# Kernel tuning notes

Measured on AMD Instinct MI355X. Metric: run time of the kernel, lower is better.

Reference implementation:

```python
import jax, jax.numpy as jnp
import numpy as np

B, V, H, W = 2, 16, 512, 512
MAX_VARS, EMBED, P = 48, 1024, 8


def setup_inputs() -> dict:
    key = jax.random.key(0)
    k1, k2, k3, k4 = jax.random.split(key, 4)
    x = jax.random.normal(k1, (B, V, H, W), dtype=jnp.float32)
    vars_idx = jax.random.randint(k2, (V,), 0, MAX_VARS)
    # params scaled roughly like kaiming_uniform for fan_in = P*P
    bound = 1.0 / np.sqrt(P * P)
    proj_weights = jax.random.normal(k3, (MAX_VARS, EMBED, 1, P, P), dtype=jnp.float32) * bound
    proj_biases = jax.random.normal(k4, (MAX_VARS, EMBED), dtype=jnp.float32) * bound
    return {"x": x, "vars": vars_idx, "proj_weights": proj_weights, "proj_biases": proj_biases}


def reference(x, vars, proj_weights, proj_biases):
    # x: [B, V, H, W]; proj_weights: [max_vars, E, 1, p, p]; proj_biases: [max_vars, E]
    b, v, h_img, w_img = x.shape
    p = proj_weights.shape[-1]
    w_sel = proj_weights[vars][:, :, 0]          # [V, E, p, p]  (weight gather)
    b_sel = proj_biases[vars]                    # [V, E]
    hh, ww = h_img // p, w_img // p
    # non-overlapping patch extraction (stride == kernel) + per-variable matmul
    xp = x.reshape(b, v, hh, p, ww, p)           # [B, V, hh, p, ww, p]
    proj = jnp.einsum('bvhpwq,vepq->bvhwe', xp, w_sel)  # [B, V, hh, ww, E]
    # flatten=True: [B, V, L, E], L = hh*ww (matches reshape->flatten(3)->transpose(2,3))
    out = proj.reshape(b, v, hh * ww, -1) + b_sel[None, :, None, :]
    return out  # norm_layer=None -> Identity
```

## Files before the change

### kernel.cpp

```cpp
#include <hip/hip_runtime.h>
#include <hip/hip_bf16.h>

#define Bb 2
#define Vv 16
#define Hh 512
#define Ww 512
#define Kk 64
#define Ee 1024
#define Ll 4096

typedef __bf16 bf16x8 __attribute__((ext_vector_type(8)));
typedef float f32x4 __attribute__((ext_vector_type(4)));

#define LDSS 72

__global__ __launch_bounds__(256) void patch_embed_kernel(
    const float* __restrict__ x, const int* __restrict__ vars,
    const float* __restrict__ pw, const float* __restrict__ pb,
    float* __restrict__ out)
{
    __shared__ __bf16 As[128 * LDSS];
    __shared__ __bf16 Bs[128 * LDSS];

    const int tid = threadIdx.x;
    const int nt  = blockIdx.x;
    const int mt  = blockIdx.y;
    const int bv  = blockIdx.z;
    const int v   = bv & (Vv - 1);
    const int var = vars[v];

    const float4* xp = (const float4*)(x + ((size_t)bv * Hh + (size_t)mt * 16) * Ww);
    #pragma unroll
    for (int i = 0; i < 8; i++) {
        int f = tid + i * 256;
        float4 val = xp[f];
        int r  = f >> 7;
        int c4 = f & 127;
        int l  = ((r >> 3) << 6) + (c4 >> 1);
        int k  = ((r & 7) << 3) + ((c4 & 1) << 2);
        __bf16* d = &As[l * LDSS + k];
        d[0] = (__bf16)val.x; d[1] = (__bf16)val.y;
        d[2] = (__bf16)val.z; d[3] = (__bf16)val.w;
    }
    const float4* wp = (const float4*)(pw + ((size_t)var * Ee + (size_t)nt * 128) * Kk);
    #pragma unroll
    for (int i = 0; i < 8; i++) {
        int f = tid + i * 256;
        float4 val = wp[f];
        int row = f >> 4;
        int k   = (f & 15) << 2;
        __bf16* d = &Bs[row * LDSS + k];
        d[0] = (__bf16)val.x; d[1] = (__bf16)val.y;
        d[2] = (__bf16)val.z; d[3] = (__bf16)val.w;
    }
    __syncthreads();

    const int lane = tid & 63;
    const int wv   = tid >> 6;
    const int wm   = (wv >> 1) << 6;
    const int wn   = (wv & 1) << 6;
    const int ln   = lane & 15;
    const int quad = lane >> 4;

    f32x4 acc[4][4] = {};
    #pragma unroll
    for (int kh = 0; kh < 2; kh++) {
        bf16x8 af[4], bfr[4];
        #pragma unroll
        for (int mi = 0; mi < 4; mi++)
            af[mi] = *(const bf16x8*)&As[(wm + mi * 16 + ln) * LDSS + kh * 32 + quad * 8];
        #pragma unroll
        for (int nj = 0; nj < 4; nj++)
            bfr[nj] = *(const bf16x8*)&Bs[(wn + nj * 16 + ln) * LDSS + kh * 32 + quad * 8];
        #pragma unroll
        for (int mi = 0; mi < 4; mi++)
            #pragma unroll
            for (int nj = 0; nj < 4; nj++)
                acc[mi][nj] = __builtin_amdgcn_mfma_f32_16x16x32_bf16(
                    af[mi], bfr[nj], acc[mi][nj], 0, 0, 0);
    }

    const float* bias = pb + (size_t)var * Ee;
    float bv4[4];
    #pragma unroll
    for (int nj = 0; nj < 4; nj++)
        bv4[nj] = bias[nt * 128 + wn + nj * 16 + ln];

    float* outp = out + (size_t)bv * Ll * Ee;
    #pragma unroll
    for (int mi = 0; mi < 4; mi++) {
        int m0 = mt * 128 + wm + mi * 16 + quad * 4;
        #pragma unroll
        for (int r = 0; r < 4; r++) {
            float* row = outp + (size_t)(m0 + r) * Ee + nt * 128 + wn + ln;
            #pragma unroll
            for (int nj = 0; nj < 4; nj++)
                row[nj * 16] = acc[mi][nj][r] + bv4[nj];
        }
    }
}

extern "C" void kernel_launch(void* const* d_in, const int* in_sizes, int n_in,
                              void* d_out, int out_size, void* d_ws, size_t ws_size,
                              hipStream_t stream) {
    const float* x    = (const float*)d_in[0];
    const int*   vars = (const int*)d_in[1];
    const float* pw   = (const float*)d_in[2];
    const float* pb   = (const float*)d_in[3];
    float* out = (float*)d_out;
    dim3 grid(Ee / 128, Ll / 128, Bb * Vv);
    dim3 block(256);
    hipLaunchKernelGGL(patch_embed_kernel, grid, block, 0, stream,
                       x, vars, pw, pb, out);
}
```

Measured before the change: 665.6 us.

## Swap MFMA operand roles to emit vectorized nontemporal float4 output stores

Swaps the MFMA operands so weights form the A side and patches the B side. Each lane's accumulator then holds four consecutive embedding columns for one output row, which allows 16-byte nontemporal vector stores in place of scalar strided stores. The change also packs LDS writes as bf16x4 and loads the bias as float4 before the barrier. The kernel is dominated by writing 512MB of output, so it targets store efficiency, with some risk from the nontemporal cache behaviour.

```diff
diff --git a/kernel.cpp b/kernel.cpp
--- a/kernel.cpp
+++ b/kernel.cpp
@@ -10,6 +10,7 @@
 #define Ll 4096
 
 typedef __bf16 bf16x8 __attribute__((ext_vector_type(8)));
+typedef __bf16 bf16x4 __attribute__((ext_vector_type(4)));
 typedef float f32x4 __attribute__((ext_vector_type(4)));
 
 #define LDSS 72
@@ -19,8 +20,8 @@
     const float* __restrict__ pw, const float* __restrict__ pb,
     float* __restrict__ out)
 {
-    __shared__ __bf16 As[128 * LDSS];
-    __shared__ __bf16 Bs[128 * LDSS];
+    __shared__ __bf16 Xs[128 * LDSS];
+    __shared__ __bf16 Wt[128 * LDSS];
 
     const int tid = threadIdx.x;
     const int nt  = blockIdx.x;
@@ -38,9 +39,8 @@
         int c4 = f & 127;
         int l  = ((r >> 3) << 6) + (c4 >> 1);
         int k  = ((r & 7) << 3) + ((c4 & 1) << 2);
-        __bf16* d = &As[l * LDSS + k];
-        d[0] = (__bf16)val.x; d[1] = (__bf16)val.y;
-        d[2] = (__bf16)val.z; d[3] = (__bf16)val.w;
+        bf16x4 pk = { (__bf16)val.x, (__bf16)val.y, (__bf16)val.z, (__bf16)val.w };
+        *(bf16x4*)&Xs[l * LDSS + k] = pk;
     }
     const float4* wp = (const float4*)(pw + ((size_t)var * Ee + (size_t)nt * 128) * Kk);
     #pragma unroll
@@ -49,53 +49,55 @@
         float4 val = wp[f];
         int row = f >> 4;
         int k   = (f & 15) << 2;
-        __bf16* d = &Bs[row * LDSS + k];
-        d[0] = (__bf16)val.x; d[1] = (__bf16)val.y;
-        d[2] = (__bf16)val.z; d[3] = (__bf16)val.w;
+        bf16x4 pk = { (__bf16)val.x, (__bf16)val.y, (__bf16)val.z, (__bf16)val.w };
+        *(bf16x4*)&Wt[row * LDSS + k] = pk;
     }
-    __syncthreads();
 
     const int lane = tid & 63;
     const int wv   = tid >> 6;
-    const int wm   = (wv >> 1) << 6;
-    const int wn   = (wv & 1) << 6;
+    const int wE   = (wv >> 1) << 6;
+    const int wL   = (wv & 1) << 6;
     const int ln   = lane & 15;
     const int quad = lane >> 4;
+
+    const float4* b4 = (const float4*)(pb + (size_t)var * Ee + nt * 128 + wE + quad * 4);
+    f32x4 bias4[4];
+    #pragma unroll
+    for (int mi = 0; mi < 4; mi++) {
+        float4 t = b4[mi * 4];
+        f32x4 u = { t.x, t.y, t.z, t.w };
+        bias4[mi] = u;
+    }
+
+    __syncthreads();
 
     f32x4 acc[4][4] = {};
     #pragma unroll
     for (int kh = 0; kh < 2; kh++) {
-        bf16x8 af[4], bfr[4];
+        bf16x8 wf[4], xf[4];
         #pragma unroll
         for (int mi = 0; mi < 4; mi++)
-            af[mi] = *(const bf16x8*)&As[(wm + mi * 16 + ln) * LDSS + kh * 32 + quad * 8];
+            wf[mi] = *(const bf16x8*)&Wt[(wE + mi * 16 + ln) * LDSS + kh * 32 + quad * 8];
         #pragma unroll
         for (int nj = 0; nj < 4; nj++)
-            bfr[nj] = *(const bf16x8*)&Bs[(wn + nj * 16 + ln) * LDSS + kh * 32 + quad * 8];
+            xf[nj] = *(const bf16x8*)&Xs[(wL + nj * 16 + ln) * LDSS + kh * 32 + quad * 8];
         #pragma unroll
         for (int mi = 0; mi < 4; mi++)
             #pragma unroll
             for (int nj = 0; nj < 4; nj++)
                 acc[mi][nj] = __builtin_amdgcn_mfma_f32_16x16x32_bf16(
-                    af[mi], bfr[nj], acc[mi][nj], 0, 0, 0);
+                    wf[mi], xf[nj], acc[mi][nj], 0, 0, 0);
     }
-
-    const float* bias = pb + (size_t)var * Ee;
-    float bv4[4];
-    #pragma unroll
-    for (int nj = 0; nj < 4; nj++)
-        bv4[nj] = bias[nt * 128 + wn + nj * 16 + ln];
 
     float* outp = out + (size_t)bv * Ll * Ee;
     #pragma unroll
-    for (int mi = 0; mi < 4; mi++) {
-        int m0 = mt * 128 + wm + mi * 16 + quad * 4;
+    for (int nj = 0; nj < 4; nj++) {
+        size_t rowoff = (size_t)(mt * 128 + wL + nj * 16 + ln) * Ee
+                      + (size_t)(nt * 128 + wE + quad * 4);
         #pragma unroll
-        for (int r = 0; r < 4; r++) {
-            float* row = outp + (size_t)(m0 + r) * Ee + nt * 128 + wn + ln;
-            #pragma unroll
-            for (int nj = 0; nj < 4; nj++)
-                row[nj * 16] = acc[mi][nj][r] + bv4[nj];
+        for (int mi = 0; mi < 4; mi++) {
+            f32x4 val = acc[mi][nj] + bias4[mi];
+            __builtin_nontemporal_store(val, (f32x4*)(outp + rowoff + mi * 16));
         }
     }
 }
```

Measured after the change: 598.3 us. 1.11x faster.
